# Performance work log

Measured on AMD Instinct MI355X. Metric: run time of the kernel, lower is better.

## Reference

```python
import jax, jax.numpy as jnp
import numpy as np

B, C, H, W = 2, 256, 64, 64
HEADS, DIM_HEAD = 8, 64
INNER = HEADS * DIM_HEAD


def setup_inputs() -> dict:
    key = jax.random.key(0)
    k1, k2, k3, k4 = jax.random.split(key, 4)
    x = jax.random.normal(k1, (B, C, H, W), dtype=jnp.float32)
    # 1x1 conv weights stored as [out_ch, in_ch]
    w_qkv = jax.random.normal(k2, (3 * INNER, C), dtype=jnp.float32) * (1.0 / np.sqrt(C))
    w_out = jax.random.normal(k3, (C, INNER), dtype=jnp.float32) * (1.0 / np.sqrt(INNER))
    b_out = jax.random.normal(k4, (C,), dtype=jnp.float32) * 0.01
    return {"x": x, "w_qkv": w_qkv, "w_out": w_out, "b_out": b_out}


def reference(x, w_qkv, w_out, b_out):
    b, c, h, w = x.shape
    n = h * w
    # 1x1 conv == channel matmul
    qkv = jnp.einsum('oc,bchw->bohw', w_qkv, x)  # [B, 3*inner, H, W]
    qkv = qkv.reshape(b, 3, HEADS, DIM_HEAD, n)
    qkv = jnp.transpose(qkv, (1, 0, 2, 4, 3))    # [3, B, heads, N, dim_head]
    q, k, v = qkv[0], qkv[1], qkv[2]
    scale = 1.0 / (DIM_HEAD ** 0.5)
    dots = jnp.einsum('bhnd,bhmd->bhnm', q, k) * scale  # [B, heads, N, N]
    attn = jax.nn.softmax(dots, axis=-1)
    out = jnp.einsum('bhnm,bhmd->bhnd', attn, v)        # [B, heads, N, dim_head]
    out = jnp.transpose(out, (0, 1, 3, 2)).reshape(b, INNER, h, w)
    return jnp.einsum('ci,bihw->bchw', w_out, out) + b_out[None, :, None, None]
```

## Files before the change

kernel.cpp:

```cpp
#include <hip/hip_runtime.h>
#include <hip/hip_bf16.h>

typedef unsigned short u16;
typedef __attribute__((ext_vector_type(8))) short bf16x8;
typedef __attribute__((ext_vector_type(4))) short bf16x4;
typedef __attribute__((ext_vector_type(4))) float f32x4;
typedef __attribute__((ext_vector_type(8))) unsigned short u16x8;
typedef __attribute__((ext_vector_type(4))) unsigned short u16x4;

#define N_POS 4096
#define HEADS 8
#define DHEAD 64
#define CIN   256
#define INNER 512

__device__ __forceinline__ u16 f2bf(float f) {
    union { float f; unsigned int u; } v; v.f = f;
    unsigned int u = v.u + 0x7FFFu + ((v.u >> 16) & 1u);
    return (u16)(u >> 16);
}

__device__ __forceinline__ unsigned int pkbf2(float lo, float hi) {
    union { __hip_bfloat162 b; unsigned int u; } cv;
    cv.b = __float22bfloat162_rn(make_float2(lo, hi));
    return cv.u;
}

__global__ __launch_bounds__(256) void k0_prep(const float* __restrict__ x,
                                               const float* __restrict__ w_qkv,
                                               const float* __restrict__ w_out,
                                               u16* __restrict__ xT,
                                               u16* __restrict__ wq,
                                               u16* __restrict__ wo) {
    int bid = blockIdx.x;
    int t   = threadIdx.x;
    if (bid < 256) {
        int b = bid >> 7, rest = bid & 127;
        int n  = (rest & 15) * 256 + t;
        int c0 = (rest >> 4) * 32;
        const float* xp = x + (size_t)b * CIN * N_POS + n;
        u16* op = xT + ((size_t)(b * N_POS + n)) * CIN + c0;
        for (int g = 0; g < 4; ++g) {
            u16x8 v;
            for (int j = 0; j < 8; ++j)
                v[j] = f2bf(xp[(size_t)(c0 + g * 8 + j) * N_POS]);
            *(u16x8*)(op + g * 8) = v;
        }
    } else if (bid < 448) {
        size_t idx = (size_t)(bid - 256) * 2048 + t * 8;
        u16x8 v;
        for (int j = 0; j < 8; ++j) v[j] = f2bf(w_qkv[idx + j]);
        *(u16x8*)(wq + idx) = v;
    } else {
        size_t idx = (size_t)(bid - 448) * 2048 + t * 8;
        u16x8 v;
        for (int j = 0; j < 8; ++j) v[j] = f2bf(w_out[idx + j]);
        *(u16x8*)(wo + idx) = v;
    }
}

__global__ __launch_bounds__(256) void k1_qkv(const u16* __restrict__ wq,
                                              const u16* __restrict__ xT,
                                              u16* __restrict__ q_ws,
                                              u16* __restrict__ k_ws,
                                              u16* __restrict__ vt_ws) {
    __shared__ u16 Alds[64 * 40];
    __shared__ u16 Blds[64 * 40];
    int tid = threadIdx.x;
    int n0  = blockIdx.x * 64;
    int by  = blockIdx.y;
    int b   = blockIdx.z;
    int o0  = by * 64;
    int sel = by >> 3;
    int h   = by & 7;
    int wv = tid >> 6, l = tid & 63, quad = l >> 4, l15 = l & 15;
    int srow = tid >> 2, sseg = tid & 3;

    f32x4 acc[4] = {};
    for (int c0 = 0; c0 < CIN; c0 += 32) {
        const u16* wp = wq + (size_t)(o0 + srow) * CIN + c0 + sseg * 8;
        *(u16x8*)&Alds[srow * 40 + sseg * 8] = *(const u16x8*)wp;
        const u16* xp = xT + ((size_t)(b * N_POS + n0 + srow)) * CIN + c0 + sseg * 8;
        *(u16x8*)&Blds[srow * 40 + sseg * 8] = *(const u16x8*)xp;
        __syncthreads();
        bf16x8 af = *(const bf16x8*)&Alds[(wv * 16 + l15) * 40 + quad * 8];
        for (int nt = 0; nt < 4; ++nt) {
            bf16x8 bfrag = *(const bf16x8*)&Blds[(nt * 16 + l15) * 40 + quad * 8];
            acc[nt] = __builtin_amdgcn_mfma_f32_16x16x32_bf16(af, bfrag, acc[nt], 0, 0, 0);
        }
        __syncthreads();
    }
    const float QSCALE = 0.125f * 1.44269504088896f;
    float sc = (sel == 0) ? QSCALE : 1.0f;
    int dbase = wv * 16 + quad * 4;
    for (int nt = 0; nt < 4; ++nt) {
        int n = n0 + nt * 16 + l15;
        if (sel < 2) {
            u16* base = (sel == 0) ? q_ws : k_ws;
            u16x4 pk;
            for (int r = 0; r < 4; ++r) pk[r] = f2bf(acc[nt][r] * sc);
            *(u16x4*)&base[((size_t)((b * HEADS + h) * N_POS + n)) * DHEAD + dbase] = pk;
        } else {
            for (int r = 0; r < 4; ++r)
                vt_ws[((size_t)((b * HEADS + h) * DHEAD + dbase + r)) * N_POS + n] =
                    f2bf(acc[nt][r]);
        }
    }
}

__global__ __launch_bounds__(256, 2) void k2_attn(const u16* __restrict__ q_ws,
                                                  const u16* __restrict__ k_ws,
                                                  const u16* __restrict__ vt_ws,
                                                  u16* __restrict__ ao_ws) {
    __shared__ u16 Klds[64 * 72];
    __shared__ u16 Vlds[64 * 72];
    int tid = threadIdx.x;
    int q0  = blockIdx.x * 128;
    int bh  = blockIdx.y;
    int wv = tid >> 6, l = tid & 63, quad = l >> 4, l15 = l & 15;
    int srow = tid >> 2, sseg = tid & 3;

    const u16* qp = q_ws + ((size_t)(bh * N_POS + q0 + wv * 32 + l15)) * DHEAD + quad * 8;
    bf16x8 bq[2][2];
    bq[0][0] = *(const bf16x8*)qp;
    bq[0][1] = *(const bf16x8*)(qp + 32);
    bq[1][0] = *(const bf16x8*)(qp + 16 * DHEAD);
    bq[1][1] = *(const bf16x8*)(qp + 16 * DHEAD + 32);

    f32x4 Oacc[2][4] = {};
    float lsum[2] = {0.f, 0.f};

    const u16* kp = k_ws + ((size_t)(bh * N_POS + srow)) * DHEAD + sseg * 16;
    const u16* vp = vt_ws + ((size_t)(bh * DHEAD + srow)) * N_POS + sseg * 16;

    u16x8 pf0 = *(const u16x8*)kp;
    u16x8 pf1 = *(const u16x8*)(kp + 8);
    u16x8 pf2 = *(const u16x8*)vp;
    u16x8 pf3 = *(const u16x8*)(vp + 8);

    for (int j0 = 0; j0 < N_POS; j0 += 64) {
        *(u16x8*)&Klds[srow * 72 + sseg * 16]     = pf0;
        *(u16x8*)&Klds[srow * 72 + sseg * 16 + 8] = pf1;
        *(u16x8*)&Vlds[srow * 72 + sseg * 16]     = pf2;
        *(u16x8*)&Vlds[srow * 72 + sseg * 16 + 8] = pf3;
        __syncthreads();

        if (j0 + 64 < N_POS) {
            const u16* kpj = kp + (size_t)(j0 + 64) * DHEAD;
            pf0 = *(const u16x8*)kpj;
            pf1 = *(const u16x8*)(kpj + 8);
            pf2 = *(const u16x8*)(vp + j0 + 64);
            pf3 = *(const u16x8*)(vp + j0 + 72);
        }

        f32x4 ST[2][4];
        for (int jt = 0; jt < 4; ++jt) {
            const u16* kb = &Klds[(jt * 16 + l15) * 72 + quad * 8];
            bf16x8 kf0 = *(const bf16x8*)kb;
            bf16x8 kf1 = *(const bf16x8*)(kb + 32);
            for (int it = 0; it < 2; ++it) {
                f32x4 z = {};
                z = __builtin_amdgcn_mfma_f32_16x16x32_bf16(kf0, bq[it][0], z, 0, 0, 0);
                z = __builtin_amdgcn_mfma_f32_16x16x32_bf16(kf1, bq[it][1], z, 0, 0, 0);
                ST[it][jt] = z;
            }
        }

        bf16x4 pk[2][4];
        for (int it = 0; it < 2; ++it) {
            float rs = 0.f;
            for (int jt = 0; jt < 4; ++jt)
                for (int r = 0; r < 4; ++r) {
                    float p = __builtin_amdgcn_exp2f(ST[it][jt][r]);
                    ST[it][jt][r] = p;
                    rs += p;
                }
            lsum[it] += rs;
            for (int jt = 0; jt < 4; ++jt) {
                union { unsigned int u[2]; bf16x4 v; } cv;
                cv.u[0] = pkbf2(ST[it][jt][0], ST[it][jt][1]);
                cv.u[1] = pkbf2(ST[it][jt][2], ST[it][jt][3]);
                pk[it][jt] = cv.v;
            }
        }

        for (int dt = 0; dt < 4; ++dt) {
            const u16* vb = &Vlds[(dt * 16 + l15) * 72 + quad * 4];
            for (int jt = 0; jt < 4; ++jt) {
                bf16x4 vf = *(const bf16x4*)(vb + jt * 16);
                Oacc[0][dt] = __builtin_amdgcn_mfma_f32_16x16x16bf16_1k(vf, pk[0][jt], Oacc[0][dt], 0, 0, 0);
                Oacc[1][dt] = __builtin_amdgcn_mfma_f32_16x16x16bf16_1k(vf, pk[1][jt], Oacc[1][dt], 0, 0, 0);
            }
        }
        __syncthreads();
    }

    int b = bh >> 3, h = bh & 7;
    for (int it = 0; it < 2; ++it) {
        float ls = lsum[it];
        ls += __shfl_xor(ls, 16);
        ls += __shfl_xor(ls, 32);
        float inv = 1.0f / ls;
        int n = q0 + wv * 32 + it * 16 + l15;
        u16* dst = ao_ws + ((size_t)(b * N_POS + n)) * INNER + h * DHEAD;
        for (int dt = 0; dt < 4; ++dt) {
            u16x4 w;
            for (int r = 0; r < 4; ++r) w[r] = f2bf(Oacc[it][dt][r] * inv);
            *(u16x4*)&dst[dt * 16 + quad * 4] = w;
        }
    }
}

__global__ __launch_bounds__(256) void k3_out(const u16* __restrict__ wo,
                                              const float* __restrict__ b_out,
                                              const u16* __restrict__ ao_ws,
                                              float* __restrict__ out) {
    __shared__ u16 Alds[64 * 40];
    __shared__ u16 Blds[64 * 40];
    int tid = threadIdx.x;
    int n0 = blockIdx.x * 64;
    int c0 = blockIdx.y * 64;
    int b  = blockIdx.z;
    int wv = tid >> 6, l = tid & 63, quad = l >> 4, l15 = l & 15;
    int srow = tid >> 2, sseg = tid & 3;

    f32x4 acc[4] = {};
    for (int i0 = 0; i0 < INNER; i0 += 32) {
        const u16* wp = wo + (size_t)(c0 + srow) * INNER + i0 + sseg * 8;
        *(u16x8*)&Alds[srow * 40 + sseg * 8] = *(const u16x8*)wp;
        const u16* bp = ao_ws + ((size_t)(b * N_POS + n0 + srow)) * INNER + i0 + sseg * 8;
        *(u16x8*)&Blds[srow * 40 + sseg * 8] = *(const u16x8*)bp;
        __syncthreads();
        bf16x8 af = *(const bf16x8*)&Alds[(wv * 16 + l15) * 40 + quad * 8];
        for (int nt = 0; nt < 4; ++nt) {
            bf16x8 bfrag = *(const bf16x8*)&Blds[(nt * 16 + l15) * 40 + quad * 8];
            acc[nt] = __builtin_amdgcn_mfma_f32_16x16x32_bf16(af, bfrag, acc[nt], 0, 0, 0);
        }
        __syncthreads();
    }
    for (int r = 0; r < 4; ++r) {
        int c = c0 + wv * 16 + quad * 4 + r;
        float bias = b_out[c];
        for (int nt = 0; nt < 4; ++nt) {
            int n = n0 + nt * 16 + l15;
            out[((size_t)(b * CIN + c)) * N_POS + n] = acc[nt][r] + bias;
        }
    }
}

extern "C" void kernel_launch(void* const* d_in, const int* in_sizes, int n_in,
                              void* d_out, int out_size, void* d_ws, size_t ws_size,
                              hipStream_t stream) {
    const float* x     = (const float*)d_in[0];
    const float* w_qkv = (const float*)d_in[1];
    const float* w_out = (const float*)d_in[2];
    const float* b_out = (const float*)d_in[3];
    float* out = (float*)d_out;

    u16* ws    = (u16*)d_ws;
    u16* xT    = ws;
    u16* q_ws  = xT   + (size_t)2 * N_POS * CIN;
    u16* k_ws  = q_ws + (size_t)2 * HEADS * N_POS * DHEAD;
    u16* vt_ws = k_ws + (size_t)2 * HEADS * N_POS * DHEAD;
    u16* ao_ws = vt_ws + (size_t)2 * HEADS * N_POS * DHEAD;
    u16* wq_bf = ao_ws + (size_t)2 * N_POS * INNER;
    u16* wo_bf = wq_bf + (size_t)3 * INNER * CIN;

    hipLaunchKernelGGL(k0_prep, dim3(512), dim3(256), 0, stream,
                       x, w_qkv, w_out, xT, wq_bf, wo_bf);
    hipLaunchKernelGGL(k1_qkv, dim3(64, 24, 2), dim3(256), 0, stream,
                       wq_bf, xT, q_ws, k_ws, vt_ws);
    hipLaunchKernelGGL(k2_attn, dim3(32, 16, 1), dim3(256), 0, stream,
                       q_ws, k_ws, vt_ws, ao_ws);
    hipLaunchKernelGGL(k3_out, dim3(64, 4, 2), dim3(256), 0, stream,
                       wo_bf, b_out, ao_ws, out);
}
```

Before: 194.7 us.

## Split attention over key range and combine partials; widen QKV projection tile

```diff
diff --git a/kernel.cpp b/kernel.cpp
--- a/kernel.cpp
+++ b/kernel.cpp
@@ -13,6 +13,8 @@
 #define DHEAD 64
 #define CIN   256
 #define INNER 512
+#define NSPLIT 2
+#define JCHUNK (N_POS / NSPLIT)
 
 __device__ __forceinline__ u16 f2bf(float f) {
     union { float f; unsigned int u; } v; v.f = f;
@@ -59,15 +61,15 @@
     }
 }
 
-__global__ __launch_bounds__(256) void k1_qkv(const u16* __restrict__ wq,
-                                              const u16* __restrict__ xT,
-                                              u16* __restrict__ q_ws,
-                                              u16* __restrict__ k_ws,
-                                              u16* __restrict__ vt_ws) {
+__global__ __launch_bounds__(256, 4) void k1_qkv(const u16* __restrict__ wq,
+                                                 const u16* __restrict__ xT,
+                                                 u16* __restrict__ q_ws,
+                                                 u16* __restrict__ k_ws,
+                                                 u16* __restrict__ vt_ws) {
     __shared__ u16 Alds[64 * 40];
-    __shared__ u16 Blds[64 * 40];
+    __shared__ u16 Blds[128 * 40];
     int tid = threadIdx.x;
-    int n0  = blockIdx.x * 64;
+    int n0  = blockIdx.x * 128;
     int by  = blockIdx.y;
     int b   = blockIdx.z;
     int o0  = by * 64;
@@ -75,16 +77,18 @@
     int h   = by & 7;
     int wv = tid >> 6, l = tid & 63, quad = l >> 4, l15 = l & 15;
     int srow = tid >> 2, sseg = tid & 3;
-
-    f32x4 acc[4] = {};
+    int brow = tid >> 1, bseg = tid & 1;
+
+    f32x4 acc[8] = {};
     for (int c0 = 0; c0 < CIN; c0 += 32) {
-        const u16* wp = wq + (size_t)(o0 + srow) * CIN + c0 + sseg * 8;
-        *(u16x8*)&Alds[srow * 40 + sseg * 8] = *(const u16x8*)wp;
-        const u16* xp = xT + ((size_t)(b * N_POS + n0 + srow)) * CIN + c0 + sseg * 8;
-        *(u16x8*)&Blds[srow * 40 + sseg * 8] = *(const u16x8*)xp;
+        *(u16x8*)&Alds[srow * 40 + sseg * 8] =
+            *(const u16x8*)(wq + (size_t)(o0 + srow) * CIN + c0 + sseg * 8);
+        const u16* xp = xT + ((size_t)(b * N_POS + n0 + brow)) * CIN + c0 + bseg * 16;
+        *(u16x8*)&Blds[brow * 40 + bseg * 16]     = *(const u16x8*)xp;
+        *(u16x8*)&Blds[brow * 40 + bseg * 16 + 8] = *(const u16x8*)(xp + 8);
         __syncthreads();
         bf16x8 af = *(const bf16x8*)&Alds[(wv * 16 + l15) * 40 + quad * 8];
-        for (int nt = 0; nt < 4; ++nt) {
+        for (int nt = 0; nt < 8; ++nt) {
             bf16x8 bfrag = *(const bf16x8*)&Blds[(nt * 16 + l15) * 40 + quad * 8];
             acc[nt] = __builtin_amdgcn_mfma_f32_16x16x32_bf16(af, bfrag, acc[nt], 0, 0, 0);
         }
@@ -93,7 +97,7 @@
     const float QSCALE = 0.125f * 1.44269504088896f;
     float sc = (sel == 0) ? QSCALE : 1.0f;
     int dbase = wv * 16 + quad * 4;
-    for (int nt = 0; nt < 4; ++nt) {
+    for (int nt = 0; nt < 8; ++nt) {
         int n = n0 + nt * 16 + l15;
         if (sel < 2) {
             u16* base = (sel == 0) ? q_ws : k_ws;
@@ -108,15 +112,18 @@
     }
 }
 
-__global__ __launch_bounds__(256, 2) void k2_attn(const u16* __restrict__ q_ws,
+__global__ __launch_bounds__(256, 4) void k2_attn(const u16* __restrict__ q_ws,
                                                   const u16* __restrict__ k_ws,
                                                   const u16* __restrict__ vt_ws,
-                                                  u16* __restrict__ ao_ws) {
+                                                  float* __restrict__ op_ws,
+                                                  float* __restrict__ lw_ws) {
     __shared__ u16 Klds[64 * 72];
     __shared__ u16 Vlds[64 * 72];
     int tid = threadIdx.x;
     int q0  = blockIdx.x * 128;
     int bh  = blockIdx.y;
+    int half = blockIdx.z;
+    int jbase = half * JCHUNK;
     int wv = tid >> 6, l = tid & 63, quad = l >> 4, l15 = l & 15;
     int srow = tid >> 2, sseg = tid & 3;
 
@@ -133,19 +140,19 @@
     const u16* kp = k_ws + ((size_t)(bh * N_POS + srow)) * DHEAD + sseg * 16;
     const u16* vp = vt_ws + ((size_t)(bh * DHEAD + srow)) * N_POS + sseg * 16;
 
-    u16x8 pf0 = *(const u16x8*)kp;
-    u16x8 pf1 = *(const u16x8*)(kp + 8);
-    u16x8 pf2 = *(const u16x8*)vp;
-    u16x8 pf3 = *(const u16x8*)(vp + 8);
-
-    for (int j0 = 0; j0 < N_POS; j0 += 64) {
+    u16x8 pf0 = *(const u16x8*)(kp + (size_t)jbase * DHEAD);
+    u16x8 pf1 = *(const u16x8*)(kp + (size_t)jbase * DHEAD + 8);
+    u16x8 pf2 = *(const u16x8*)(vp + jbase);
+    u16x8 pf3 = *(const u16x8*)(vp + jbase + 8);
+
+    for (int j0 = jbase; j0 < jbase + JCHUNK; j0 += 64) {
         *(u16x8*)&Klds[srow * 72 + sseg * 16]     = pf0;
         *(u16x8*)&Klds[srow * 72 + sseg * 16 + 8] = pf1;
         *(u16x8*)&Vlds[srow * 72 + sseg * 16]     = pf2;
         *(u16x8*)&Vlds[srow * 72 + sseg * 16 + 8] = pf3;
         __syncthreads();
 
-        if (j0 + 64 < N_POS) {
+        if (j0 + 64 < jbase + JCHUNK) {
             const u16* kpj = kp + (size_t)(j0 + 64) * DHEAD;
             pf0 = *(const u16x8*)kpj;
             pf1 = *(const u16x8*)(kpj + 8);
@@ -196,19 +203,44 @@
     }
 
     int b = bh >> 3, h = bh & 7;
+    float* opb = op_ws + (size_t)half * 2 * N_POS * INNER;
+    float* lwb = lw_ws + (size_t)half * 2 * HEADS * N_POS;
     for (int it = 0; it < 2; ++it) {
         float ls = lsum[it];
         ls += __shfl_xor(ls, 16);
         ls += __shfl_xor(ls, 32);
-        float inv = 1.0f / ls;
         int n = q0 + wv * 32 + it * 16 + l15;
-        u16* dst = ao_ws + ((size_t)(b * N_POS + n)) * INNER + h * DHEAD;
-        for (int dt = 0; dt < 4; ++dt) {
-            u16x4 w;
-            for (int r = 0; r < 4; ++r) w[r] = f2bf(Oacc[it][dt][r] * inv);
-            *(u16x4*)&dst[dt * 16 + quad * 4] = w;
-        }
-    }
+        if (quad == 0) lwb[(size_t)bh * N_POS + n] = ls;
+        float* dst = opb + ((size_t)(b * N_POS + n)) * INNER + h * DHEAD;
+        for (int dt = 0; dt < 4; ++dt)
+            *(f32x4*)&dst[dt * 16 + quad * 4] = Oacc[it][dt];
+    }
+}
+
+__global__ __launch_bounds__(256) void k2c_combine(const float* __restrict__ op_ws,
+                                                   const float* __restrict__ lw_ws,
+                                                   u16* __restrict__ ao_ws) {
+    size_t gid = (size_t)blockIdx.x * 256 + threadIdx.x;
+    size_t e0  = gid * 16;
+    int i0 = (int)(e0 & (INNER - 1));
+    size_t nf = e0 >> 9;
+    int h = i0 >> 6;
+    size_t b = nf >> 12;
+    size_t n = nf & (N_POS - 1);
+    size_t lidx = (b * HEADS + h) * N_POS + n;
+    float ls = lw_ws[lidx] + lw_ws[(size_t)2 * HEADS * N_POS + lidx];
+    float inv = 1.0f / ls;
+    const float* p0 = op_ws + e0;
+    const float* p1 = op_ws + (size_t)2 * N_POS * INNER + e0;
+    u16x8 o[2];
+    for (int g = 0; g < 2; ++g) {
+        for (int k = 0; k < 8; ++k) {
+            int idx = g * 8 + k;
+            o[g][k] = f2bf((p0[idx] + p1[idx]) * inv);
+        }
+    }
+    *(u16x8*)(ao_ws + e0)     = o[0];
+    *(u16x8*)(ao_ws + e0 + 8) = o[1];
 }
 
 __global__ __launch_bounds__(256) void k3_out(const u16* __restrict__ wo,
@@ -226,10 +258,10 @@
 
     f32x4 acc[4] = {};
     for (int i0 = 0; i0 < INNER; i0 += 32) {
-        const u16* wp = wo + (size_t)(c0 + srow) * INNER + i0 + sseg * 8;
-        *(u16x8*)&Alds[srow * 40 + sseg * 8] = *(const u16x8*)wp;
-        const u16* bp = ao_ws + ((size_t)(b * N_POS + n0 + srow)) * INNER + i0 + sseg * 8;
-        *(u16x8*)&Blds[srow * 40 + sseg * 8] = *(const u16x8*)bp;
+        *(u16x8*)&Alds[srow * 40 + sseg * 8] =
+            *(const u16x8*)(wo + (size_t)(c0 + srow) * INNER + i0 + sseg * 8);
+        *(u16x8*)&Blds[srow * 40 + sseg * 8] =
+            *(const u16x8*)(ao_ws + ((size_t)(b * N_POS + n0 + srow)) * INNER + i0 + sseg * 8);
         __syncthreads();
         bf16x8 af = *(const bf16x8*)&Alds[(wv * 16 + l15) * 40 + quad * 8];
         for (int nt = 0; nt < 4; ++nt) {
@@ -265,13 +297,17 @@
     u16* ao_ws = vt_ws + (size_t)2 * HEADS * N_POS * DHEAD;
     u16* wq_bf = ao_ws + (size_t)2 * N_POS * INNER;
     u16* wo_bf = wq_bf + (size_t)3 * INNER * CIN;
+    float* op_ws = (float*)(wo_bf + (size_t)CIN * INNER);
+    float* lw_ws = op_ws + (size_t)NSPLIT * 2 * N_POS * INNER;
 
     hipLaunchKernelGGL(k0_prep, dim3(512), dim3(256), 0, stream,
                        x, w_qkv, w_out, xT, wq_bf, wo_bf);
-    hipLaunchKernelGGL(k1_qkv, dim3(64, 24, 2), dim3(256), 0, stream,
+    hipLaunchKernelGGL(k1_qkv, dim3(32, 24, 2), dim3(256), 0, stream,
                        wq_bf, xT, q_ws, k_ws, vt_ws);
-    hipLaunchKernelGGL(k2_attn, dim3(32, 16, 1), dim3(256), 0, stream,
-                       q_ws, k_ws, vt_ws, ao_ws);
+    hipLaunchKernelGGL(k2_attn, dim3(32, 16, NSPLIT), dim3(256), 0, stream,
+                       q_ws, k_ws, vt_ws, op_ws, lw_ws);
+    hipLaunchKernelGGL(k2c_combine, dim3((2 * N_POS * INNER) / (256 * 16)), dim3(256), 0, stream,
+                       op_ws, lw_ws, ao_ws);
     hipLaunchKernelGGL(k3_out, dim3(64, 4, 2), dim3(256), 0, stream,
                        wo_bf, b_out, ao_ws, out);
 }
```

Measured after the change: 193.9 us. About the same (-0.4%).
